# Performance work log

Hardware: AMD Instinct MI355X
Metric: run time of the kernel (lower is better)

The kernel has to match this reference:

```python
import jax, jax.numpy as jnp
import numpy as np
from math import sqrt

B, TS_D, SEG, D, H = 16, 2, 1024, 256, 8
D_FF = 1024
DK = D // H
EPS = 1e-5


def _layernorm(x, g, b):
    mu = jnp.mean(x, axis=-1, keepdims=True)
    var = jnp.mean(jnp.square(x - mu), axis=-1, keepdims=True)
    return (x - mu) * jax.lax.rsqrt(var + EPS) * g + b


def setup_inputs() -> dict:
    key = jax.random.key(0)
    ks = jax.random.split(key, 16)
    s = 0.02
    return {
        "x": jax.random.normal(ks[0], (B, TS_D, SEG, D), dtype=jnp.float32),
        "Wq": jax.random.normal(ks[1], (D, D), dtype=jnp.float32) * s,
        "bq": jnp.zeros((D,), jnp.float32),
        "Wk": jax.random.normal(ks[2], (D, D), dtype=jnp.float32) * s,
        "bk": jnp.zeros((D,), jnp.float32),
        "Wv": jax.random.normal(ks[3], (D, D), dtype=jnp.float32) * s,
        "bv": jnp.zeros((D,), jnp.float32),
        "Wo": jax.random.normal(ks[4], (D, D), dtype=jnp.float32) * s,
        "bo": jnp.zeros((D,), jnp.float32),
        "g31": jnp.ones((D,), jnp.float32),
        "b31": jnp.zeros((D,), jnp.float32),
        "W1": jax.random.normal(ks[5], (D, D_FF), dtype=jnp.float32) * s,
        "b1": jnp.zeros((D_FF,), jnp.float32),
        "W2": jax.random.normal(ks[6], (D_FF, D), dtype=jnp.float32) * s,
        "b2": jnp.zeros((D,), jnp.float32),
        "g41": jnp.ones((D,), jnp.float32),
        "b41": jnp.zeros((D,), jnp.float32),
    }


def reference(x, Wq, bq, Wk, bk, Wv, bv, Wo, bo, g31, b31, W1, b1, W2, b2, g41, b41):
    # x: [B, ts_d=2, seg, d]; output is final_out2 (only live path of the module)
    b, ts_d, seg, d = x.shape
    scale = 1.0 / sqrt(DK)
    segments = x.reshape(b, ts_d * seg, d)            # [B, 2*seg, d]
    Q = (segments @ Wq + bq).reshape(b, -1, H, DK)
    K = (segments @ Wk + bk).reshape(b, -1, H, DK)
    V = (segments @ Wv + bv).reshape(b, -1, H, DK)
    q = Q[:, :seg]       # first seg positions (channel 0)
    k = K[:, -seg:]      # last seg positions (channel 1)
    v = V[:, -seg:]
    # cross-segment dual attention
    A1 = jax.nn.softmax(scale * jnp.einsum('blhe,bshe->bhls', q, k), axis=-1)
    out1 = jnp.einsum('bhls,bshd->blhd', A1, v).reshape(b, seg, d)
    A2 = jax.nn.softmax(scale * jnp.einsum('blhe,bshe->bhls', k, q), axis=-1)
    out2 = jnp.einsum('bhls,bshd->blhd', A2, q).reshape(b, seg, d)
    y = jnp.concatenate([out1, out2], axis=1) @ Wo + bo   # [B, 2*seg, d]
    h = _layernorm(segments + y, g31, b31)
    mlp = jax.nn.gelu(h @ W1 + b1, approximate=False) @ W2 + b2
    h = _layernorm(h + mlp, g41, b41)
    return h.reshape(b, ts_d, seg, d)
```

## Files before the change

kernel.cpp:

```cpp
#include <hip/hip_runtime.h>
#include <hip/hip_bf16.h>
#include <math.h>

#define BATCH 16
#define SEG 1024
#define DMODEL 256
#define NH 8
#define DK 32
#define DFF 1024
#define NTOK (BATCH * 2 * SEG)
#define EPS 1e-5f

typedef __attribute__((ext_vector_type(8))) short short8;
typedef __attribute__((ext_vector_type(4))) float f32x4;

__device__ __forceinline__ ushort f2bf(float x) {
    union { float f; unsigned u; } a; a.f = x;
    unsigned r = a.u + 0x7fffu + ((a.u >> 16) & 1u);
    return (ushort)(r >> 16);
}

typedef const __attribute__((address_space(1))) unsigned gas_u32;
typedef __attribute__((address_space(3))) unsigned las_u32;
__device__ __forceinline__ void gload_lds16(const ushort* g, ushort* l) {
    __builtin_amdgcn_global_load_lds((gas_u32*)g, (las_u32*)l, 16, 0, 0);
}

__global__ __launch_bounds__(256) void wfrag_kernel(
    const float* __restrict__ src, ushort* __restrict__ dst, int K, int N, int order)
{
    const int tid = blockIdx.x * 256 + threadIdx.x;
    const int KT_ = K >> 5, NT_ = N >> 4;
    const int total = KT_ * NT_ * 64;
    if (tid >= total) return;
    const int lane = tid & 63;
    const int frag = tid >> 6;
    int kt, nt;
    if (order) { kt = frag / NT_; nt = frag % NT_; }
    else       { nt = frag / KT_; kt = frag % KT_; }
    const int quad = lane >> 4, l = lane & 15;
    const float* s = src + (size_t)(kt * 32 + quad * 8) * N + nt * 16 + l;
    short8 v;
#pragma unroll
    for (int j = 0; j < 8; j++) v[j] = (short)f2bf(s[(size_t)j * N]);
    *(short8*)&dst[(size_t)tid * 8] = v;
}

#define ASTR 264

__device__ __forceinline__ void dense256_pass(
    const ushort* __restrict__ Wf, ushort* WL, const short8* af,
    f32x4* acc, int t, int w, int lane)
{
#pragma unroll
    for (int nt = 0; nt < 16; ++nt) acc[nt] = (f32x4){0.f, 0.f, 0.f, 0.f};
    for (int c = 0; c < 4; ++c) {
        const ushort* g = Wf + (size_t)c * 16384 + w * 4096 + lane * 8;
        ushort* ld = WL + w * 4096;
#pragma unroll
        for (int i = 0; i < 8; ++i) gload_lds16(g + i * 512, ld + i * 512);
        __syncthreads();
#pragma unroll
        for (int n2 = 0; n2 < 4; ++n2)
#pragma unroll
            for (int kt = 0; kt < 8; ++kt) {
                const short8 bf_ = *(const short8*)&WL[(n2 * 8 + kt) * 512 + lane * 8];
                acc[c * 4 + n2] = __builtin_amdgcn_mfma_f32_16x16x32_bf16(af[kt], bf_, acc[c * 4 + n2], 0, 0, 0);
            }
        __syncthreads();
    }
}

__global__ __launch_bounds__(256) void qkv_mfma_kernel(
    const float* __restrict__ x,
    const ushort* __restrict__ Wqf, const float* __restrict__ bq,
    const ushort* __restrict__ Wkf, const float* __restrict__ bk,
    const ushort* __restrict__ Wvf, const float* __restrict__ bv,
    ushort* __restrict__ qbuf, ushort* __restrict__ kbuf,
    ushort* __restrict__ qt, ushort* __restrict__ vt)
{
    __shared__ __align__(16) ushort SM[64 * ASTR];
    const int bid = blockIdx.x;
    const int half = bid >> 8;
    const int sub = bid & 255;
    const int b = sub >> 4, ti = sub & 15;
    const int t = threadIdx.x;
    const int w = t >> 6, lane = t & 63, l = lane & 15, quad = lane >> 4;

    const float* xrow = x + ((size_t)b * 2048 + (size_t)half * 1024 + ti * 64) * 256;
#pragma unroll
    for (int p = 0; p < 16; ++p) {
        int ch = t + 256 * p;
        int row = ch >> 6, c4 = ch & 63;
        float4 v = *(const float4*)&xrow[row * 256 + c4 * 4];
        uint2 pk;
        pk.x = (unsigned)f2bf(v.x) | ((unsigned)f2bf(v.y) << 16);
        pk.y = (unsigned)f2bf(v.z) | ((unsigned)f2bf(v.w) << 16);
        *(uint2*)&SM[row * ASTR + c4 * 4] = pk;
    }
    __syncthreads();

    short8 af[8];
#pragma unroll
    for (int kt = 0; kt < 8; ++kt)
        af[kt] = *(const short8*)&SM[(w * 16 + l) * ASTR + kt * 32 + quad * 8];
    __syncthreads();

    f32x4 acc[16];
    const int npass = half ? 2 : 1;
    for (int pass = 0; pass < npass; ++pass) {
        const ushort* Wf = half ? (pass ? Wvf : Wkf) : Wqf;
        const float* bias = half ? (pass ? bv : bk) : bq;
        dense256_pass(Wf, SM, af, acc, t, w, lane);

        ushort bfv[16][4];
#pragma unroll
        for (int nt = 0; nt < 16; ++nt) {
            const float bb = bias[nt * 16 + l];
#pragma unroll
            for (int r = 0; r < 4; ++r) bfv[nt][r] = f2bf(acc[nt][r] + bb);
        }

        const bool rowout = (half == 0) || (pass == 0);
        const bool trout  = (half == 0) || (pass == 1);
        if (rowout) {
            ushort* obuf = half ? kbuf : qbuf;
#pragma unroll
            for (int nt = 0; nt < 16; ++nt) {
                const int h = nt >> 1, e = (nt & 1) * 16 + l;
#pragma unroll
                for (int r = 0; r < 4; ++r) {
                    int tok = ti * 64 + w * 16 + quad * 4 + r;
                    obuf[(((size_t)b * 8 + h) * SEG + tok) * 32 + e] = bfv[nt][r];
                }
            }
        }
        if (trout) {
            ushort* tb = half ? vt : qt;
#pragma unroll
            for (int nt = 0; nt < 16; ++nt)
#pragma unroll
                for (int r = 0; r < 4; ++r)
                    SM[(nt * 16 + l) * 66 + w * 16 + quad * 4 + r] = bfv[nt][r];
            __syncthreads();
            const int d = t, hh = t >> 5, e = t & 31;
            ushort* dr = tb + (((size_t)b * 8 + hh) * 32 + e) * 1024 + ti * 64;
#pragma unroll
            for (int j = 0; j < 8; ++j) {
                uint2 v;
                v.x = *(const unsigned*)&SM[d * 66 + j * 8];
                v.y = *(const unsigned*)&SM[d * 66 + j * 8 + 2];
                unsigned z0 = *(const unsigned*)&SM[d * 66 + j * 8 + 4];
                unsigned z1 = *(const unsigned*)&SM[d * 66 + j * 8 + 6];
                *(uint4*)&dr[j * 8] = make_uint4(v.x, v.y, z0, z1);
            }
        }
    }
}

#define KT 128
#define KP 40
#define VP 136
#define PP 136

__global__ __launch_bounds__(256) void attn_mfma_kernel(
    const ushort* __restrict__ qbuf, const ushort* __restrict__ kbuf,
    const ushort* __restrict__ qt, const ushort* __restrict__ vt,
    ushort* __restrict__ abuf)
{
    __shared__ __align__(16) ushort Kl[KT * KP];
    __shared__ __align__(16) ushort Vl[32 * VP];
    __shared__ __align__(16) ushort Pl[4 * 16 * PP];

    const int bid   = blockIdx.x;
    const int qtile = bid & 15;
    const int h     = (bid >> 4) & 7;
    const int b     = (bid >> 7) & 15;
    const int stage = bid >> 11;

    const ushort* Qm = stage ? kbuf : qbuf;
    const ushort* Km = stage ? qbuf : kbuf;
    const ushort* Vt = stage ? qt : vt;
    const size_t bh = ((size_t)b * 8 + h) * SEG * 32;

    const int t    = threadIdx.x;
    const int w    = t >> 6;
    const int lane = t & 63;
    const int l    = lane & 15;
    const int quad = lane >> 4;

    const int qrow = qtile * 64 + w * 16 + l;
    const short8 qf = *(const short8*)&Qm[bh + (size_t)qrow * 32 + quad * 8];

    f32x4 o0 = {0.f, 0.f, 0.f, 0.f};
    f32x4 o1 = {0.f, 0.f, 0.f, 0.f};
    float l_r[4] = {0.f, 0.f, 0.f, 0.f};
    const float scale = 0.17677669529663687f;

    ushort* Pw = &Pl[w * 16 * PP];

    for (int tile = 0; tile < 8; ++tile) {
        __syncthreads();
        const ushort* Kg = &Km[bh + (size_t)(tile * KT) * 32];
#pragma unroll
        for (int p = 0; p < 2; ++p) {
            int ch = t + 256 * p;
            int row = ch & 127, part = ch >> 7;
            *(short8*)&Kl[row * KP + part * 8] = *(const short8*)&Kg[row * 32 + part * 8];
        }
        const ushort* Vg = &Vt[bh + (size_t)tile * KT];
#pragma unroll
        for (int p = 0; p < 2; ++p) {
            int ch = t + 256 * p;
            int d = ch >> 4, c = ch & 15;
            *(short8*)&Vl[d * VP + c * 8] = *(const short8*)&Vg[(size_t)d * 1024 + c * 8];
        }
        __syncthreads();

        f32x4 sc[8];
#pragma unroll
        for (int kb = 0; kb < 8; ++kb) {
            const short8 kf = *(const short8*)&Kl[(kb * 16 + l) * KP + quad * 8];
            f32x4 z = {0.f, 0.f, 0.f, 0.f};
            sc[kb] = __builtin_amdgcn_mfma_f32_16x16x32_bf16(qf, kf, z, 0, 0, 0);
        }

#pragma unroll
        for (int kb = 0; kb < 8; ++kb)
#pragma unroll
            for (int r = 0; r < 4; ++r) {
                float p = __expf(sc[kb][r] * scale);
                l_r[r] += p;
                union { float f; unsigned u; } pu; pu.f = p;
                Pw[(quad * 4 + r) * PP + kb * 16 + l] = (ushort)((pu.u + 0x8000u) >> 16);
            }

#pragma unroll
        for (int kc = 0; kc < 4; ++kc) {
            const short8 pf  = *(const short8*)&Pw[l * PP + kc * 32 + quad * 8];
            const short8 vf0 = *(const short8*)&Vl[l * VP + kc * 32 + quad * 8];
            const short8 vf1 = *(const short8*)&Vl[(16 + l) * VP + kc * 32 + quad * 8];
            o0 = __builtin_amdgcn_mfma_f32_16x16x32_bf16(pf, vf0, o0, 0, 0, 0);
            o1 = __builtin_amdgcn_mfma_f32_16x16x32_bf16(pf, vf1, o1, 0, 0, 0);
        }
    }

#pragma unroll
    for (int r = 0; r < 4; ++r) {
        float s = l_r[r];
        s += __shfl_xor(s, 1); s += __shfl_xor(s, 2);
        s += __shfl_xor(s, 4); s += __shfl_xor(s, 8);
        float invl = 1.0f / s;
        int qo = qtile * 64 + w * 16 + quad * 4 + r;
        size_t base = ((size_t)b * 2 * SEG + (size_t)stage * SEG + qo) * 256 + h * 32;
        abuf[base + l]      = f2bf(o0[r] * invl);
        abuf[base + 16 + l] = f2bf(o1[r] * invl);
    }
}

__global__ __launch_bounds__(256) void proj_mfma_kernel(
    const ushort* __restrict__ abuf, const ushort* __restrict__ Wof,
    const float* __restrict__ bo, const float* __restrict__ x,
    const float* __restrict__ g31, const float* __restrict__ b31,
    float* __restrict__ hout, ushort* __restrict__ hbf)
{
    __shared__ __align__(16) ushort SM[64 * ASTR];
    const int bid = blockIdx.x;
    const size_t tok0 = (size_t)bid * 64;
    const int t = threadIdx.x;
    const int w = t >> 6, lane = t & 63, l = lane & 15, quad = lane >> 4;

#pragma unroll
    for (int p = 0; p < 8; ++p) {
        int ch = t + 256 * p;
        int row = ch >> 5, c8 = ch & 31;
        *(short8*)&SM[row * ASTR + c8 * 8] = *(const short8*)&abuf[(tok0 + row) * 256 + c8 * 8];
    }
    __syncthreads();

    short8 af[8];
#pragma unroll
    for (int kt = 0; kt < 8; ++kt)
        af[kt] = *(const short8*)&SM[(w * 16 + l) * ASTR + kt * 32 + quad * 8];
    __syncthreads();

    f32x4 acc[16];
    dense256_pass(Wof, SM, af, acc, t, w, lane);

#pragma unroll
    for (int nt = 0; nt < 16; ++nt) {
        const int d = nt * 16 + l;
        const float bv = bo[d];
#pragma unroll
        for (int r = 0; r < 4; ++r) {
            size_t tok = tok0 + w * 16 + quad * 4 + r;
            acc[nt][r] += bv + x[tok * 256 + d];
        }
    }

    float mu_[4], is_[4];
#pragma unroll
    for (int r = 0; r < 4; ++r) {
        float s = 0.f;
#pragma unroll
        for (int nt = 0; nt < 16; ++nt) s += acc[nt][r];
        s += __shfl_xor(s, 1); s += __shfl_xor(s, 2);
        s += __shfl_xor(s, 4); s += __shfl_xor(s, 8);
        float mu = s * (1.0f / 256.0f);
        float vs = 0.f;
#pragma unroll
        for (int nt = 0; nt < 16; ++nt) { float dd = acc[nt][r] - mu; vs += dd * dd; }
        vs += __shfl_xor(vs, 1); vs += __shfl_xor(vs, 2);
        vs += __shfl_xor(vs, 4); vs += __shfl_xor(vs, 8);
        mu_[r] = mu;
        is_[r] = rsqrtf(vs * (1.0f / 256.0f) + EPS);
    }

#pragma unroll
    for (int nt = 0; nt < 16; ++nt) {
        const int d = nt * 16 + l;
        const float gg = g31[d], bb = b31[d];
#pragma unroll
        for (int r = 0; r < 4; ++r) {
            size_t tok = tok0 + w * 16 + quad * 4 + r;
            float v = (acc[nt][r] - mu_[r]) * is_[r] * gg + bb;
            hout[tok * 256 + d] = v;
            hbf[tok * 256 + d] = f2bf(v);
        }
    }
}

#define GP 40

__global__ __launch_bounds__(256) void mlp_mfma_kernel(
    const ushort* __restrict__ hbf, const ushort* __restrict__ W1f,
    const float* __restrict__ b1, const ushort* __restrict__ W2f,
    const float* __restrict__ b2, const float* __restrict__ g41,
    const float* __restrict__ b41, float* __restrict__ io)
{
    __shared__ __align__(16) ushort SM[64 * ASTR];
    __shared__ __align__(16) ushort G[4][16 * GP];
    const int bid = blockIdx.x;
    const size_t tok0 = (size_t)bid * 64;
    const int t = threadIdx.x;
    const int w = t >> 6, lane = t & 63, l = lane & 15, quad = lane >> 4;

#pragma unroll
    for (int p = 0; p < 8; ++p) {
        int ch = t + 256 * p;
        int row = ch >> 5, c8 = ch & 31;
        *(short8*)&SM[row * ASTR + c8 * 8] = *(const short8*)&hbf[(tok0 + row) * 256 + c8 * 8];
    }
    __syncthreads();

    short8 af[8];
#pragma unroll
    for (int kt = 0; kt < 8; ++kt)
        af[kt] = *(const short8*)&SM[(w * 16 + l) * ASTR + kt * 32 + quad * 8];
    __syncthreads();

    f32x4 out[16];
#pragma unroll
    for (int nt = 0; nt < 16; ++nt) out[nt] = (f32x4){0.f, 0.f, 0.f, 0.f};

    ushort* WL = &SM[0];
    ushort* Gw = &G[w][0];

    for (int c = 0; c < 32; ++c) {
        {
            const ushort* g1 = W1f + (size_t)c * 8192 + w * 2048 + lane * 8;
            ushort* l1 = WL + w * 2048;
            const ushort* g2 = W2f + (size_t)c * 8192 + w * 2048 + lane * 8;
            ushort* l2 = WL + 8192 + w * 2048;
#pragma unroll
            for (int i = 0; i < 4; ++i) {
                gload_lds16(g1 + i * 512, l1 + i * 512);
                gload_lds16(g2 + i * 512, l2 + i * 512);
            }
        }
        __syncthreads();

        f32x4 s[2];
        s[0] = (f32x4){0.f, 0.f, 0.f, 0.f};
        s[1] = (f32x4){0.f, 0.f, 0.f, 0.f};
#pragma unroll
        for (int n2 = 0; n2 < 2; ++n2)
#pragma unroll
            for (int kt = 0; kt < 8; ++kt) {
                const short8 bf_ = *(const short8*)&WL[(n2 * 8 + kt) * 512 + lane * 8];
                s[n2] = __builtin_amdgcn_mfma_f32_16x16x32_bf16(af[kt], bf_, s[n2], 0, 0, 0);
            }

#pragma unroll
        for (int n2 = 0; n2 < 2; ++n2) {
            const int ff = (c * 2 + n2) * 16 + l;
            const float bv = b1[ff];
#pragma unroll
            for (int r = 0; r < 4; ++r) {
                float v = s[n2][r] + bv;
                float gl = 0.5f * v * (1.0f + erff(v * 0.70710678118654752f));
                Gw[(quad * 4 + r) * GP + n2 * 16 + l] = f2bf(gl);
            }
        }

        const short8 gf = *(const short8*)&Gw[l * GP + quad * 8];
#pragma unroll
        for (int nt = 0; nt < 16; ++nt) {
            const short8 bf_ = *(const short8*)&WL[8192 + nt * 512 + lane * 8];
            out[nt] = __builtin_amdgcn_mfma_f32_16x16x32_bf16(gf, bf_, out[nt], 0, 0, 0);
        }
        __syncthreads();
    }

#pragma unroll
    for (int nt = 0; nt < 16; ++nt) {
        const int d = nt * 16 + l;
        const float bv = b2[d];
#pragma unroll
        for (int r = 0; r < 4; ++r) {
            size_t tok = tok0 + w * 16 + quad * 4 + r;
            out[nt][r] += bv + io[tok * 256 + d];
        }
    }

    float mu_[4], is_[4];
#pragma unroll
    for (int r = 0; r < 4; ++r) {
        float s = 0.f;
#pragma unroll
        for (int nt = 0; nt < 16; ++nt) s += out[nt][r];
        s += __shfl_xor(s, 1); s += __shfl_xor(s, 2);
        s += __shfl_xor(s, 4); s += __shfl_xor(s, 8);
        float mu = s * (1.0f / 256.0f);
        float vs = 0.f;
#pragma unroll
        for (int nt = 0; nt < 16; ++nt) { float dd = out[nt][r] - mu; vs += dd * dd; }
        vs += __shfl_xor(vs, 1); vs += __shfl_xor(vs, 2);
        vs += __shfl_xor(vs, 4); vs += __shfl_xor(vs, 8);
        mu_[r] = mu;
        is_[r] = rsqrtf(vs * (1.0f / 256.0f) + EPS);
    }

#pragma unroll
    for (int nt = 0; nt < 16; ++nt) {
        const int d = nt * 16 + l;
        const float gg = g41[d], bb = b41[d];
#pragma unroll
        for (int r = 0; r < 4; ++r) {
            size_t tok = tok0 + w * 16 + quad * 4 + r;
            io[tok * 256 + d] = (out[nt][r] - mu_[r]) * is_[r] * gg + bb;
        }
    }
}

extern "C" void kernel_launch(void* const* d_in, const int* in_sizes, int n_in,
                              void* d_out, int out_size, void* d_ws, size_t ws_size,
                              hipStream_t stream)
{
    const float* x   = (const float*)d_in[0];
    const float* Wq  = (const float*)d_in[1];
    const float* bq  = (const float*)d_in[2];
    const float* Wk  = (const float*)d_in[3];
    const float* bk  = (const float*)d_in[4];
    const float* Wv  = (const float*)d_in[5];
    const float* bv  = (const float*)d_in[6];
    const float* Wo  = (const float*)d_in[7];
    const float* bo  = (const float*)d_in[8];
    const float* g31 = (const float*)d_in[9];
    const float* b31 = (const float*)d_in[10];
    const float* W1  = (const float*)d_in[11];
    const float* b1  = (const float*)d_in[12];
    const float* W2  = (const float*)d_in[13];
    const float* b2  = (const float*)d_in[14];
    const float* g41 = (const float*)d_in[15];
    const float* b41 = (const float*)d_in[16];

    float* out = (float*)d_out;

    const size_t HALF = (size_t)BATCH * SEG * DMODEL;
    ushort* qbuf = (ushort*)d_ws;
    ushort* kbuf = qbuf + HALF;
    ushort* qt   = kbuf + HALF;
    ushort* vt   = qt + HALF;
    ushort* abuf = vt + HALF;
    ushort* hbf  = abuf + 2 * HALF;
    ushort* Wqf  = hbf + 2 * HALF;
    ushort* Wkf  = Wqf + 65536;
    ushort* Wvf  = Wkf + 65536;
    ushort* Wof  = Wvf + 65536;
    ushort* W1f  = Wof + 65536;
    ushort* W2f  = W1f + 262144;

    wfrag_kernel<<<32, 256, 0, stream>>>(Wq, Wqf, 256, 256, 0);
    wfrag_kernel<<<32, 256, 0, stream>>>(Wk, Wkf, 256, 256, 0);
    wfrag_kernel<<<32, 256, 0, stream>>>(Wv, Wvf, 256, 256, 0);
    wfrag_kernel<<<32, 256, 0, stream>>>(Wo, Wof, 256, 256, 0);
    wfrag_kernel<<<128, 256, 0, stream>>>(W1, W1f, 256, 1024, 0);
    wfrag_kernel<<<128, 256, 0, stream>>>(W2, W2f, 1024, 256, 1);

    qkv_mfma_kernel<<<512, 256, 0, stream>>>(x, Wqf, bq, Wkf, bk, Wvf, bv,
                                             qbuf, kbuf, qt, vt);
    attn_mfma_kernel<<<2 * BATCH * NH * (SEG / 64), 256, 0, stream>>>(qbuf, kbuf, qt, vt, abuf);
    proj_mfma_kernel<<<NTOK / 64, 256, 0, stream>>>(abuf, Wof, bo, x, g31, b31, out, hbf);
    mlp_mfma_kernel<<<NTOK / 64, 256, 0, stream>>>(hbf, W1f, b1, W2f, b2, g41, b41, out);
}
```

Measured before the change: 331.6 us.

## Keep attention probabilities in registers via transposed MFMA, drop LDS P buffer

Computes scores as K·Q^T so each lane's accumulator column maps directly to the B operand of a 16x16x16 bf16 MFMA for P·V. This removes the LDS round trip for the probability matrix. It also folds the scale into exp2, reduces the row sum with two shuffles, and stages the output through LDS to emit 16-byte coalesced stores. Block index order changes so that q-tiles are the slowest-varying dimension, and the K tile load mapping is made row-contiguous. The tradeoff is that the smaller MFMA shape is used for P·V.

```diff
diff --git a/kernel.cpp b/kernel.cpp
--- a/kernel.cpp
+++ b/kernel.cpp
@@ -12,6 +12,7 @@
 #define EPS 1e-5f
 
 typedef __attribute__((ext_vector_type(8))) short short8;
+typedef __attribute__((ext_vector_type(4))) short short4b;
 typedef __attribute__((ext_vector_type(4))) float f32x4;
 
 __device__ __forceinline__ ushort f2bf(float x) {
@@ -158,25 +159,24 @@
     }
 }
 
-#define KT 128
+#define KTILE 128
 #define KP 40
 #define VP 136
-#define PP 136
 
 __global__ __launch_bounds__(256) void attn_mfma_kernel(
     const ushort* __restrict__ qbuf, const ushort* __restrict__ kbuf,
     const ushort* __restrict__ qt, const ushort* __restrict__ vt,
     ushort* __restrict__ abuf)
 {
-    __shared__ __align__(16) ushort Kl[KT * KP];
+    __shared__ __align__(16) ushort Kl[KTILE * KP];
     __shared__ __align__(16) ushort Vl[32 * VP];
-    __shared__ __align__(16) ushort Pl[4 * 16 * PP];
 
     const int bid   = blockIdx.x;
-    const int qtile = bid & 15;
-    const int h     = (bid >> 4) & 7;
-    const int b     = (bid >> 7) & 15;
-    const int stage = bid >> 11;
+    const int sbh   = bid & 255;
+    const int qtile = bid >> 8;
+    const int stage = sbh >> 7;
+    const int b     = (sbh >> 3) & 15;
+    const int h     = sbh & 7;
 
     const ushort* Qm = stage ? kbuf : qbuf;
     const ushort* Km = stage ? qbuf : kbuf;
@@ -194,21 +194,19 @@
 
     f32x4 o0 = {0.f, 0.f, 0.f, 0.f};
     f32x4 o1 = {0.f, 0.f, 0.f, 0.f};
-    float l_r[4] = {0.f, 0.f, 0.f, 0.f};
-    const float scale = 0.17677669529663687f;
-
-    ushort* Pw = &Pl[w * 16 * PP];
+    float lsum = 0.f;
+    const float SC2 = 0.25503486f;
 
     for (int tile = 0; tile < 8; ++tile) {
         __syncthreads();
-        const ushort* Kg = &Km[bh + (size_t)(tile * KT) * 32];
+        const ushort* Kg = &Km[bh + (size_t)(tile * KTILE) * 32];
 #pragma unroll
         for (int p = 0; p < 2; ++p) {
             int ch = t + 256 * p;
-            int row = ch & 127, part = ch >> 7;
+            int row = ch >> 2, part = ch & 3;
             *(short8*)&Kl[row * KP + part * 8] = *(const short8*)&Kg[row * 32 + part * 8];
         }
-        const ushort* Vg = &Vt[bh + (size_t)tile * KT];
+        const ushort* Vg = &Vt[bh + (size_t)tile * KTILE];
 #pragma unroll
         for (int p = 0; p < 2; ++p) {
             int ch = t + 256 * p;
@@ -217,45 +215,43 @@
         }
         __syncthreads();
 
-        f32x4 sc[8];
 #pragma unroll
         for (int kb = 0; kb < 8; ++kb) {
             const short8 kf = *(const short8*)&Kl[(kb * 16 + l) * KP + quad * 8];
             f32x4 z = {0.f, 0.f, 0.f, 0.f};
-            sc[kb] = __builtin_amdgcn_mfma_f32_16x16x32_bf16(qf, kf, z, 0, 0, 0);
-        }
-
-#pragma unroll
-        for (int kb = 0; kb < 8; ++kb)
+            f32x4 sc = __builtin_amdgcn_mfma_f32_16x16x32_bf16(kf, qf, z, 0, 0, 0);
+            short4b pf;
 #pragma unroll
             for (int r = 0; r < 4; ++r) {
-                float p = __expf(sc[kb][r] * scale);
-                l_r[r] += p;
-                union { float f; unsigned u; } pu; pu.f = p;
-                Pw[(quad * 4 + r) * PP + kb * 16 + l] = (ushort)((pu.u + 0x8000u) >> 16);
-            }
-
-#pragma unroll
-        for (int kc = 0; kc < 4; ++kc) {
-            const short8 pf  = *(const short8*)&Pw[l * PP + kc * 32 + quad * 8];
-            const short8 vf0 = *(const short8*)&Vl[l * VP + kc * 32 + quad * 8];
-            const short8 vf1 = *(const short8*)&Vl[(16 + l) * VP + kc * 32 + quad * 8];
-            o0 = __builtin_amdgcn_mfma_f32_16x16x32_bf16(pf, vf0, o0, 0, 0, 0);
-            o1 = __builtin_amdgcn_mfma_f32_16x16x32_bf16(pf, vf1, o1, 0, 0, 0);
-        }
-    }
-
+                float p = exp2f(sc[r] * SC2);
+                lsum += p;
+                pf[r] = (short)f2bf(p);
+            }
+            const short4b vf0 = *(const short4b*)&Vl[l * VP + kb * 16 + quad * 4];
+            const short4b vf1 = *(const short4b*)&Vl[(16 + l) * VP + kb * 16 + quad * 4];
+            o0 = __builtin_amdgcn_mfma_f32_16x16x16bf16_1k(vf0, pf, o0, 0, 0, 0);
+            o1 = __builtin_amdgcn_mfma_f32_16x16x16bf16_1k(vf1, pf, o1, 0, 0, 0);
+        }
+    }
+
+    lsum += __shfl_xor(lsum, 16);
+    lsum += __shfl_xor(lsum, 32);
+    const float inv = 1.0f / lsum;
+#pragma unroll
+    for (int r = 0; r < 4; ++r) { o0[r] *= inv; o1[r] *= inv; }
+
+    __syncthreads();
+    ushort* Ob = &Kl[w * 16 * 40];
 #pragma unroll
     for (int r = 0; r < 4; ++r) {
-        float s = l_r[r];
-        s += __shfl_xor(s, 1); s += __shfl_xor(s, 2);
-        s += __shfl_xor(s, 4); s += __shfl_xor(s, 8);
-        float invl = 1.0f / s;
-        int qo = qtile * 64 + w * 16 + quad * 4 + r;
-        size_t base = ((size_t)b * 2 * SEG + (size_t)stage * SEG + qo) * 256 + h * 32;
-        abuf[base + l]      = f2bf(o0[r] * invl);
-        abuf[base + 16 + l] = f2bf(o1[r] * invl);
-    }
+        Ob[l * 40 + quad * 4 + r]      = f2bf(o0[r]);
+        Ob[l * 40 + 16 + quad * 4 + r] = f2bf(o1[r]);
+    }
+    __syncthreads();
+    const int q = lane >> 2, part = lane & 3;
+    const short8 ov = *(const short8*)&Ob[q * 40 + part * 8];
+    const int tok = qtile * 64 + w * 16 + q;
+    *(short8*)&abuf[((size_t)b * 2 * SEG + (size_t)stage * SEG + tok) * 256 + h * 32 + part * 8] = ov;
 }
 
 __global__ __launch_bounds__(256) void proj_mfma_kernel(
```

New measurement: 333.7 us. Within noise of the previous version (+0.6%).
